# Performance work log

Hardware: AMD Instinct MI355X
Metric: run time of the kernel (lower is better)

The kernel has to match this reference:

```python
import jax, jax.numpy as jnp
import numpy as np

B, D, H, NSTEPS = 4096, 512, 2048, 16


def setup_inputs() -> dict:
    key = jax.random.key(0)
    k1, k2, k3, k4 = jax.random.split(key, 4)
    s_x = 1.0 / np.sqrt(D)
    s_h = 1.0 / np.sqrt(H)
    return {
        "z_in": jax.random.normal(k1, (B, D), dtype=jnp.float32),
        "Wx": jax.random.normal(k2, (D, H), dtype=jnp.float32) * s_x,
        "Wh": jax.random.normal(k3, (H, H), dtype=jnp.float32) * s_h,
        "bh": jnp.zeros((H,), dtype=jnp.float32),
        "Wout": jax.random.normal(k4, (H, D), dtype=jnp.float32) * s_h,
        "bout": jnp.zeros((D,), dtype=jnp.float32),
        "n_steps": NSTEPS,
    }


def reference(z_in, Wx, Wh, bh, Wout, bout, n_steps):
    # Input projection is identical every step (same z_in fed each iteration).
    xproj = z_in @ Wx + bh  # [B, H]
    h0 = jnp.zeros((z_in.shape[0], Wh.shape[0]), dtype=z_in.dtype)

    def step(h, _):
        h_new = jnp.tanh(xproj + h @ Wh)          # Elman RNN cell, hidden retained
        out = h_new @ Wout + bout                  # MLP head hidden -> latent
        return h_new, out

    _, outs = jax.lax.scan(step, h0, None, length=n_steps)  # [n_steps, B, D]
    return jnp.transpose(outs, (1, 0, 2))  # torch.stack(outs, 1) -> [B, n_steps, D]
```

## Files before the change

kernel.cpp:

```cpp
#include <hip/hip_runtime.h>
#include <hip/hip_bf16.h>
#include <stdint.h>

#define B_ 4096
#define D_ 512
#define H_ 2048
#define NS_ 16

typedef __bf16 bf16x8 __attribute__((ext_vector_type(8)));
typedef float f32x4 __attribute__((ext_vector_type(4)));
typedef short short4v __attribute__((ext_vector_type(4)));
typedef __attribute__((address_space(3))) const bf16x8* lds_frag_p;

__device__ __forceinline__ short f2bf(float f) {
  union { float f; uint32_t u; } c; c.f = f;
  uint32_t u = c.u;
  return (short)((u + 0x7fffu + ((u >> 16) & 1u)) >> 16);
}

__device__ __forceinline__ float tanh_fast(float x) {
  float e = __expf(2.0f * x);
  return 1.0f - 2.0f / (e + 1.0f);
}

__device__ __forceinline__ void gload16(const void* g, void* l) {
  __builtin_amdgcn_global_load_lds((const __attribute__((address_space(1))) void*)g,
                                   (__attribute__((address_space(3))) void*)l,
                                   16, 0, 0);
}

__global__ __launch_bounds__(256, 5) void fused_step(
    const short* __restrict__ A, const short* __restrict__ Bt, int K,
    const float* __restrict__ xproj, const float* __restrict__ bias,
    float* __restrict__ outf, short* __restrict__ outh, int tout)
{
  __shared__ short lds[2 * 6144];
  const int tid = threadIdx.x, lane = tid & 63, wid = tid >> 6;
  const int wm = wid >> 1, wn = wid & 1;
  const int NT = K >> 5;

  const int i = (int)blockIdx.x >> 3;
  const int tn = ((int)blockIdx.x & 7) * 5 + (i % 5);
  const int tm = i / 5;
  const int row0 = tm * 128, col0 = tn * 64;

  const int r0 = wid * 16 + (lane >> 2);
  const int r1 = r0 + 64;
  const int sl = lane & 3;
  const short* gA0 = A  + (size_t)(row0 + r0) * K + ((sl ^ ((r0 >> 1) & 3)) << 3);
  const short* gA1 = A  + (size_t)(row0 + r1) * K + ((sl ^ ((r1 >> 1) & 3)) << 3);
  const short* gB0 = Bt + (size_t)(col0 + r0) * K + ((sl ^ ((r0 >> 1) & 3)) << 3);
  const int dls = r0 * 32 + sl * 8;

  auto stage = [&](int kt, int base) {
    const size_t ko = (size_t)kt * 32;
    gload16(gA0 + ko, &lds[base + dls]);
    gload16(gA1 + ko, &lds[base + 2048 + dls]);
    gload16(gB0 + ko, &lds[base + 4096 + dls]);
  };

  const int rr = lane & 15, s4 = lane >> 4;
  int offA[4], offB[2];
#pragma unroll
  for (int m = 0; m < 4; ++m) {
    int r = wm * 64 + m * 16 + rr;
    offA[m] = r * 32 + ((s4 ^ ((r >> 1) & 3)) << 3);
  }
#pragma unroll
  for (int n = 0; n < 2; ++n) {
    int r = wn * 32 + n * 16 + rr;
    offB[n] = 4096 + r * 32 + ((s4 ^ ((r >> 1) & 3)) << 3);
  }

  f32x4 acc[4][2];
#pragma unroll
  for (int m = 0; m < 4; ++m)
#pragma unroll
    for (int n = 0; n < 2; ++n)
      acc[m][n] = (f32x4){0.f, 0.f, 0.f, 0.f};

  stage(0, 0);
  __syncthreads();
  for (int kt = 0; kt < NT; ++kt) {
    if (kt + 1 < NT) stage(kt + 1, ((kt + 1) & 1) * 6144);
    const int bb = (kt & 1) * 6144;
    bf16x8 a[4], b[2];
#pragma unroll
    for (int m = 0; m < 4; ++m) a[m] = *(lds_frag_p)&lds[bb + offA[m]];
#pragma unroll
    for (int n = 0; n < 2; ++n) b[n] = *(lds_frag_p)&lds[bb + offB[n]];
#pragma unroll
    for (int m = 0; m < 4; ++m)
#pragma unroll
      for (int n = 0; n < 2; ++n)
        acc[m][n] = __builtin_amdgcn_mfma_f32_16x16x32_bf16(a[m], b[n], acc[m][n], 0, 0, 0);
    __syncthreads();
  }

  const int rb = row0 + wm * 64 + (s4 << 2);
  const int cb = col0 + wn * 32 + rr;
  if (col0 < H_) {
#pragma unroll
    for (int m = 0; m < 4; ++m) {
#pragma unroll
      for (int n = 0; n < 2; ++n) {
        const int col = cb + n * 16;
#pragma unroll
        for (int r = 0; r < 4; ++r) {
          const int row = rb + m * 16 + r;
          float x = xproj[(size_t)row * H_ + col];
          outh[(size_t)row * H_ + col] = f2bf(tanh_fast(x + acc[m][n][r]));
        }
      }
    }
  } else {
#pragma unroll
    for (int m = 0; m < 4; ++m) {
#pragma unroll
      for (int n = 0; n < 2; ++n) {
        const int oc = cb - H_ + n * 16;
#pragma unroll
        for (int r = 0; r < 4; ++r) {
          const int row = rb + m * 16 + r;
          outf[(size_t)row * (NS_ * D_) + tout * D_ + oc] = acc[m][n][r] + bias[oc];
        }
      }
    }
  }
}

template<int BM, int BN, int EPI>
__global__ __launch_bounds__(256, 2) void gemm_bt(
    const short* __restrict__ A, const short* __restrict__ Bt, int K,
    const float* __restrict__ xproj, const float* __restrict__ bias,
    float* __restrict__ outf, short* __restrict__ outh, int ldN, int tout)
{
  constexpr int WM = BM / 2, WN = BN / 2;
  constexpr int RM = WM / 16, RN = WN / 16;
  __shared__ short lds[2][(BM + BN) * 32];
  const int tid = threadIdx.x, lane = tid & 63, wid = tid >> 6;
  const int wm = wid >> 1, wn = wid & 1;
  const int row0 = blockIdx.y * BM, col0 = blockIdx.x * BN;
  const short* Ag = A + (size_t)row0 * K;
  const short* Bg = Bt + (size_t)col0 * K;

  f32x4 acc[RM][RN];
#pragma unroll
  for (int m = 0; m < RM; ++m)
#pragma unroll
    for (int n = 0; n < RN; ++n)
      acc[m][n] = (f32x4){0.f, 0.f, 0.f, 0.f};

  const int nt = K >> 5;

  auto stage = [&](int kt, int buf) {
    const short* ga = Ag + (kt << 5);
#pragma unroll
    for (int i = 0; i < BM * 4; i += 256) {
      int slot = i + tid;
      gload16(ga + (size_t)(slot >> 2) * K + ((slot & 3) << 3), &lds[buf][slot * 8]);
    }
    const short* gb = Bg + (kt << 5);
#pragma unroll
    for (int i = 0; i < BN * 4; i += 256) {
      int slot = i + tid;
      gload16(gb + (size_t)(slot >> 2) * K + ((slot & 3) << 3),
              &lds[buf][BM * 32 + slot * 8]);
    }
  };

  stage(0, 0);
  __syncthreads();
  int cur = 0;
  const int kq = (lane >> 4) << 3;
  const int rr = lane & 15;
  for (int kt = 0; kt < nt; ++kt) {
    if (kt + 1 < nt) stage(kt + 1, cur ^ 1);
    const short* la = &lds[cur][(wm * WM) * 32];
    const short* lb = &lds[cur][BM * 32 + (wn * WN) * 32];
    bf16x8 a[RM], b[RN];
#pragma unroll
    for (int m = 0; m < RM; ++m)
      a[m] = *(const bf16x8*)(la + (m * 16 + rr) * 32 + kq);
#pragma unroll
    for (int n = 0; n < RN; ++n)
      b[n] = *(const bf16x8*)(lb + (n * 16 + rr) * 32 + kq);
#pragma unroll
    for (int m = 0; m < RM; ++m)
#pragma unroll
      for (int n = 0; n < RN; ++n)
        acc[m][n] = __builtin_amdgcn_mfma_f32_16x16x32_bf16(a[m], b[n], acc[m][n], 0, 0, 0);
    __syncthreads();
    cur ^= 1;
  }

  const int rb = row0 + wm * WM + ((lane >> 4) << 2);
  const int cb = col0 + wn * WN + (lane & 15);
#pragma unroll
  for (int m = 0; m < RM; ++m) {
#pragma unroll
    for (int n = 0; n < RN; ++n) {
      const int col = cb + n * 16;
#pragma unroll
      for (int r = 0; r < 4; ++r) {
        const int row = rb + m * 16 + r;
        float v = acc[m][n][r];
        if (EPI == 0) {
          outf[(size_t)row * ldN + col] = v + bias[col];
        } else {
          outf[(size_t)row * (NS_ * D_) + tout * D_ + col] = v + bias[col];
        }
      }
    }
  }
}

__global__ void transpose_cvt(const float* __restrict__ in, short* __restrict__ out,
                              int R, int C) {
  __shared__ float tile[32][33];
  const int tx = threadIdx.x & 31, ty = threadIdx.x >> 5;
  const int c0 = blockIdx.x * 32, r0 = blockIdx.y * 32;
#pragma unroll
  for (int i = 0; i < 32; i += 8)
    tile[ty + i][tx] = in[(size_t)(r0 + ty + i) * C + c0 + tx];
  __syncthreads();
#pragma unroll
  for (int i = 0; i < 32; i += 8)
    out[(size_t)(c0 + ty + i) * R + r0 + tx] = f2bf(tile[tx][ty + i]);
}

__global__ void cvt_bf16_k(const float4* __restrict__ in, short4v* __restrict__ out, int n4) {
  int i = blockIdx.x * 256 + threadIdx.x;
  if (i >= n4) return;
  float4 v = in[i];
  short4v o;
  o[0] = f2bf(v.x); o[1] = f2bf(v.y); o[2] = f2bf(v.z); o[3] = f2bf(v.w);
  out[i] = o;
}

__global__ void tanh_h0_k(const float4* __restrict__ xp, short4v* __restrict__ h, int n4) {
  int i = blockIdx.x * 256 + threadIdx.x;
  if (i >= n4) return;
  float4 v = xp[i];
  short4v o;
  o[0] = f2bf(tanh_fast(v.x)); o[1] = f2bf(tanh_fast(v.y));
  o[2] = f2bf(tanh_fast(v.z)); o[3] = f2bf(tanh_fast(v.w));
  h[i] = o;
}

extern "C" void kernel_launch(void* const* d_in, const int* in_sizes, int n_in,
                              void* d_out, int out_size, void* d_ws, size_t ws_size,
                              hipStream_t stream) {
  const float* z    = (const float*)d_in[0];
  const float* Wx   = (const float*)d_in[1];
  const float* Wh   = (const float*)d_in[2];
  const float* bh   = (const float*)d_in[3];
  const float* Wout = (const float*)d_in[4];
  const float* bout = (const float*)d_in[5];
  float* out = (float*)d_out;

  short* zb    = (short*)d_ws;
  short* WxT   = zb + (size_t)B_ * D_;
  short* WcatT = WxT + (size_t)H_ * D_;
  short* WoutT = WcatT + (size_t)H_ * H_;
  short* h0    = WcatT + (size_t)(H_ + D_) * H_;
  short* h1    = h0 + (size_t)B_ * H_;
  float* xproj = (float*)(h1 + (size_t)B_ * H_);

  cvt_bf16_k<<<(B_ * D_ / 4 + 255) / 256, 256, 0, stream>>>((const float4*)z, (short4v*)zb, B_ * D_ / 4);
  transpose_cvt<<<dim3(H_ / 32, D_ / 32), 256, 0, stream>>>(Wx, WxT, D_, H_);
  transpose_cvt<<<dim3(H_ / 32, H_ / 32), 256, 0, stream>>>(Wh, WcatT, H_, H_);
  transpose_cvt<<<dim3(D_ / 32, H_ / 32), 256, 0, stream>>>(Wout, WoutT, H_, D_);

  gemm_bt<128, 128, 0><<<dim3(H_ / 128, B_ / 128), 256, 0, stream>>>(
      zb, WxT, D_, nullptr, bh, xproj, nullptr, H_, 0);
  tanh_h0_k<<<(B_ * H_ / 4 + 255) / 256, 256, 0, stream>>>((const float4*)xproj, (short4v*)h0, B_ * H_ / 4);

  short* hb[2] = {h0, h1};
  for (int t = 1; t <= 15; ++t) {
    const short* hp = hb[(t - 1) & 1];
    short* hn = hb[t & 1];
    fused_step<<<1280, 256, 0, stream>>>(
        hp, WcatT, H_, xproj, bout, out, hn, t - 1);
  }
  gemm_bt<128, 64, 2><<<dim3(D_ / 64, B_ / 128), 256, 0, stream>>>(
      hb[1], WoutT, H_, nullptr, bout, out, nullptr, 0, 15);
}
```

Before: 1.199 ms.

## Restructure recurrent step kernel into single-wave 64x64 tiles without barriers

```diff
diff --git a/kernel.cpp b/kernel.cpp
--- a/kernel.cpp
+++ b/kernel.cpp
@@ -29,81 +29,88 @@
                                    16, 0, 0);
 }
 
-__global__ __launch_bounds__(256, 5) void fused_step(
+__global__ __launch_bounds__(64, 8) void fused_step(
     const short* __restrict__ A, const short* __restrict__ Bt, int K,
     const float* __restrict__ xproj, const float* __restrict__ bias,
     float* __restrict__ outf, short* __restrict__ outh, int tout)
 {
-  __shared__ short lds[2 * 6144];
-  const int tid = threadIdx.x, lane = tid & 63, wid = tid >> 6;
-  const int wm = wid >> 1, wn = wid & 1;
+  __shared__ short lds[2 * 4096];
+  const int lane = threadIdx.x;
   const int NT = K >> 5;
 
   const int i = (int)blockIdx.x >> 3;
   const int tn = ((int)blockIdx.x & 7) * 5 + (i % 5);
   const int tm = i / 5;
-  const int row0 = tm * 128, col0 = tn * 64;
-
-  const int r0 = wid * 16 + (lane >> 2);
-  const int r1 = r0 + 64;
+  const int row0 = tm * 64, col0 = tn * 64;
+
+  const int sr = lane >> 2;
   const int sl = lane & 3;
-  const short* gA0 = A  + (size_t)(row0 + r0) * K + ((sl ^ ((r0 >> 1) & 3)) << 3);
-  const short* gA1 = A  + (size_t)(row0 + r1) * K + ((sl ^ ((r1 >> 1) & 3)) << 3);
-  const short* gB0 = Bt + (size_t)(col0 + r0) * K + ((sl ^ ((r0 >> 1) & 3)) << 3);
-  const int dls = r0 * 32 + sl * 8;
-
-  auto stage = [&](int kt, int base) {
+  const short* gA[4]; const short* gB[4];
+#pragma unroll
+  for (int s = 0; s < 4; ++s) {
+    int r = s * 16 + sr;
+    gA[s] = A  + (size_t)(row0 + r) * K + ((sl ^ ((r >> 1) & 3)) << 3);
+    gB[s] = Bt + (size_t)(col0 + r) * K + ((sl ^ ((r >> 1) & 3)) << 3);
+  }
+  const int dls = sr * 32 + sl * 8;
+
+  auto stage = [&](int kt) {
+    const int base = (kt & 1) * 4096;
     const size_t ko = (size_t)kt * 32;
-    gload16(gA0 + ko, &lds[base + dls]);
-    gload16(gA1 + ko, &lds[base + 2048 + dls]);
-    gload16(gB0 + ko, &lds[base + 4096 + dls]);
+#pragma unroll
+    for (int s = 0; s < 4; ++s)
+      gload16(gA[s] + ko, &lds[base + s * 512 + dls]);
+#pragma unroll
+    for (int s = 0; s < 4; ++s)
+      gload16(gB[s] + ko, &lds[base + 2048 + s * 512 + dls]);
   };
 
   const int rr = lane & 15, s4 = lane >> 4;
-  int offA[4], offB[2];
+  int offA[4], offB[4];
 #pragma unroll
   for (int m = 0; m < 4; ++m) {
-    int r = wm * 64 + m * 16 + rr;
+    int r = m * 16 + rr;
     offA[m] = r * 32 + ((s4 ^ ((r >> 1) & 3)) << 3);
-  }
-#pragma unroll
-  for (int n = 0; n < 2; ++n) {
-    int r = wn * 32 + n * 16 + rr;
-    offB[n] = 4096 + r * 32 + ((s4 ^ ((r >> 1) & 3)) << 3);
-  }
-
-  f32x4 acc[4][2];
+    offB[m] = 2048 + r * 32 + ((s4 ^ ((r >> 1) & 3)) << 3);
+  }
+
+  f32x4 acc[4][4];
 #pragma unroll
   for (int m = 0; m < 4; ++m)
 #pragma unroll
-    for (int n = 0; n < 2; ++n)
+    for (int n = 0; n < 4; ++n)
       acc[m][n] = (f32x4){0.f, 0.f, 0.f, 0.f};
 
-  stage(0, 0);
-  __syncthreads();
+  stage(0);
   for (int kt = 0; kt < NT; ++kt) {
-    if (kt + 1 < NT) stage(kt + 1, ((kt + 1) & 1) * 6144);
-    const int bb = (kt & 1) * 6144;
-    bf16x8 a[4], b[2];
+    if (kt + 1 < NT) {
+      stage(kt + 1);
+      asm volatile("s_waitcnt vmcnt(8)" ::: "memory");
+    } else {
+      asm volatile("s_waitcnt vmcnt(0)" ::: "memory");
+    }
+    const int bb = (kt & 1) * 4096;
+    bf16x8 a[4], b[4];
 #pragma unroll
     for (int m = 0; m < 4; ++m) a[m] = *(lds_frag_p)&lds[bb + offA[m]];
 #pragma unroll
-    for (int n = 0; n < 2; ++n) b[n] = *(lds_frag_p)&lds[bb + offB[n]];
+    for (int n = 0; n < 4; ++n) b[n] = *(lds_frag_p)&lds[bb + offB[n]];
+    __builtin_amdgcn_s_setprio(1);
 #pragma unroll
     for (int m = 0; m < 4; ++m)
 #pragma unroll
-      for (int n = 0; n < 2; ++n)
+      for (int n = 0; n < 4; ++n)
         acc[m][n] = __builtin_amdgcn_mfma_f32_16x16x32_bf16(a[m], b[n], acc[m][n], 0, 0, 0);
-    __syncthreads();
-  }
-
-  const int rb = row0 + wm * 64 + (s4 << 2);
-  const int cb = col0 + wn * 32 + rr;
+    __builtin_amdgcn_s_setprio(0);
+  }
+
+  const int rb = row0 + s4 * 4;
+  const int cb = col0 + rr;
   if (col0 < H_) {
 #pragma unroll
     for (int m = 0; m < 4; ++m) {
 #pragma unroll
-      for (int n = 0; n < 2; ++n) {
+      for (int n = 0; n < 4; ++n) {
         const int col = cb + n * 16;
 #pragma unroll
         for (int r = 0; r < 4; ++r) {
@@ -117,7 +124,7 @@
 #pragma unroll
     for (int m = 0; m < 4; ++m) {
 #pragma unroll
-      for (int n = 0; n < 2; ++n) {
+      for (int n = 0; n < 4; ++n) {
         const int oc = cb - H_ + n * 16;
 #pragma unroll
         for (int r = 0; r < 4; ++r) {
@@ -280,7 +287,7 @@
   for (int t = 1; t <= 15; ++t) {
     const short* hp = hb[(t - 1) & 1];
     short* hn = hb[t & 1];
-    fused_step<<<1280, 256, 0, stream>>>(
+    fused_step<<<2560, 64, 0, stream>>>(
         hp, WcatT, H_, xproj, bout, out, hn, t - 1);
   }
   gemm_bt<128, 64, 2><<<dim3(D_ / 64, B_ / 128), 256, 0, stream>>>(
```

New measurement: 1.604 ms. +33.8%, slower.
